# Kernel optimization log

Measured on AMD Instinct MI355X. Metric: run time of the kernel, lower is better.

The kernel has to match this reference:

```python
import jax, jax.numpy as jnp
import numpy as np

N_NODES = 100000


def gcn_conv(x, row, col, W, b, n_nodes):
    # PyG GCNConv: add self-loops, symmetric normalization, linear, scatter-add, bias
    deg = jnp.zeros((n_nodes,), x.dtype).at[col].add(1.0)
    dinv = jnp.where(deg > 0, jax.lax.rsqrt(deg), 0.0)
    norm = dinv[row] * dinv[col]                      # [E+N]
    h = x @ W                                         # [N, out]
    msg = h[row] * norm[:, None]                      # [E+N, out]
    out = jax.ops.segment_sum(msg, col, num_segments=n_nodes)
    return out + b


def setup_inputs() -> dict:
    key = jax.random.key(0)
    ks = jax.random.split(key, 8)
    E = 1600000
    edge_index = jax.random.randint(ks[0], (2, E), 0, N_NODES, dtype=jnp.int64)
    node_features = jax.random.normal(ks[1], (N_NODES, 16), dtype=jnp.float32)
    W1 = jax.random.normal(ks[2], (16, 32), dtype=jnp.float32) * 0.25
    b1 = jnp.zeros((32,), jnp.float32)
    W2 = jax.random.normal(ks[3], (32, 16), dtype=jnp.float32) * 0.18
    b2 = jnp.zeros((16,), jnp.float32)
    fc_W = jax.random.normal(ks[4], (16, 1), dtype=jnp.float32) * 0.25
    fc_b = jnp.zeros((1,), jnp.float32)
    return {"edge_index": edge_index, "node_features": node_features,
            "W1": W1, "b1": b1, "W2": W2, "b2": b2, "fc_W": fc_W, "fc_b": fc_b}


def reference(edge_index, node_features, W1, b1, W2, b2, fc_W, fc_b):
    n = node_features.shape[0]
    loops = jnp.arange(n, dtype=edge_index.dtype)
    row = jnp.concatenate([edge_index[0], loops])     # sources (with self-loops)
    col = jnp.concatenate([edge_index[1], loops])     # targets (with self-loops)
    x = jax.nn.relu(gcn_conv(node_features, row, col, W1, b1, n))
    # F.dropout with training=False is identity (inference)
    x = jax.nn.relu(gcn_conv(x, row, col, W2, b2, n))
    return x @ fc_W + fc_b
```

## Files before the change

### kernel.cpp

```cpp
#include <hip/hip_runtime.h>
#include <hip/hip_fp16.h>


constexpr int NN  = 100000;
constexpr int FIN = 16;
constexpr int FH  = 32;
constexpr int FO  = 16;

constexpr int BK      = 256;
constexpr int NBUCKET = (NN + BK - 1) / BK;
constexpr int CHUNK   = 8192;
constexpr int CAP     = 5632;

static __device__ __forceinline__ int pack2(float a, float b) {
    __half2 t = __float22half2_rn(make_float2(a, b));
    return *reinterpret_cast<int*>(&t);
}
static __device__ __forceinline__ float2 unpack2(int v) {
    __half2 t = *reinterpret_cast<__half2*>(&v);
    return __half22float2(t);
}

__global__ void init_kernel(int* __restrict__ bcursor,
                            __half* __restrict__ g1, __half* __restrict__ g2) {
    int b = blockIdx.x * blockDim.x + threadIdx.x;
    if (b < NBUCKET) bcursor[b] = b * CAP;
    if (b < 4) ((int4*)(g1 + (long long)NN * FH))[b] = make_int4(0, 0, 0, 0);
    else if (b < 6) ((int4*)(g2 + (long long)NN * FO))[b - 4] = make_int4(0, 0, 0, 0);
}

__global__ __launch_bounds__(512) void bucket_fill_kernel(
        const int* __restrict__ row, const int* __restrict__ col,
        int* __restrict__ bcursor, int* __restrict__ srow, int E) {
    __shared__ int bcnt[NBUCKET];
    __shared__ int bcur[NBUCKET];
    int t = threadIdx.x;
    int e0 = blockIdx.x * CHUNK;
    int m = E - e0; if (m > CHUNK) m = CHUNK;
    for (int b = t; b < NBUCKET; b += 512) bcnt[b] = 0;
    __syncthreads();
    for (int i = t; i < m; i += 512)
        atomicAdd(&bcnt[col[e0 + i] >> 8], 1);
    __syncthreads();
    for (int b = t; b < NBUCKET; b += 512) {
        int v = bcnt[b];
        bcur[b] = v ? atomicAdd(&bcursor[b], v) : 0;
    }
    __syncthreads();
    for (int i = t; i < m; i += 512) {
        int c = col[e0 + i];
        int r = row[e0 + i];
        int p = atomicAdd(&bcur[c >> 8], 1);
        srow[p] = ((c & (BK - 1)) << 17) | r;
    }
}

__global__ __launch_bounds__(512) void bucket_sort_mm1_kernel(
        const int* __restrict__ bcursor, int* __restrict__ srow,
        int* __restrict__ off, int* __restrict__ cnt, float* __restrict__ dinv,
        const float* __restrict__ x, const float* __restrict__ W1,
        __half* __restrict__ g1, int n) {
    __shared__ int ebuf[CAP];
    __shared__ int sorted[CAP];
    __shared__ int cnt2[BK];
    __shared__ float sdi[BK];
    __shared__ int wsum[4];
    __shared__ int wbase[4];
    __shared__ int Mtot;
    __shared__ float w1[FIN * FH];
    int t = threadIdx.x;
    for (int i = t; i < FIN * FH; i += 512) w1[i] = W1[i];
    int lo = blockIdx.x << 8;
    int nodes = n - lo; if (nodes > BK) nodes = BK;
    int s0 = blockIdx.x * CAP;
    int m = bcursor[blockIdx.x] - s0;
    if (m > CAP) m = CAP;
    if (m < 0)  m = 0;
    for (int i = t; i < m; i += 512) ebuf[i] = srow[s0 + i];
    if (t < BK) cnt2[t] = 0;
    __syncthreads();
    for (int i = t; i < m; i += 512) atomicAdd(&cnt2[ebuf[i] >> 17], 1);
    __syncthreads();
    int v = 0, pv = 0, s = 0, excl = 0;
    if (t < BK) {
        v  = cnt2[t];
        pv = (v + 3) & ~3;
        s  = pv;
        #pragma unroll
        for (int d = 1; d < 64; d <<= 1) {
            int u = __shfl_up(s, d, 64);
            if ((t & 63) >= d) s += u;
        }
        if ((t & 63) == 63) wsum[t >> 6] = s;
    }
    __syncthreads();
    if (t < 4) {
        int b = 0;
        for (int k = 0; k < t; k++) b += wsum[k];
        wbase[t] = b;
    }
    __syncthreads();
    if (t < BK) {
        excl = s + wbase[t >> 6] - pv;
        cnt2[t] = excl;
        float di = rsqrtf((float)v + 1.0f);
        sdi[t] = di;
        if (t < nodes) {
            off[lo + t]  = s0 + excl;
            cnt[lo + t]  = v;
            dinv[lo + t] = di;
        }
        if (t == BK - 1) Mtot = excl + pv;
    }
    __syncthreads();
    for (int i = t; i < m; i += 512) {
        int pvv = ebuf[i];
        int p = atomicAdd(&cnt2[pvv >> 17], 1);
        sorted[p] = pvv & 0x1FFFF;
    }
    __syncthreads();
    if (t < BK) {
        for (int p = excl + v; p < excl + pv; p++) sorted[p] = NN;
    }
    __syncthreads();
    int M = Mtot; if (M > CAP) M = CAP;
    for (int i = t; i < M; i += 512) srow[s0 + i] = sorted[i];
    int lane = t >> 8;
    int nd0  = t & 255;
    if (nd0 < nodes) {
        int nd = lo + nd0;
        float di = sdi[nd0];
        float xi[FIN];
        const float4* xv = (const float4*)(x + (long long)nd * FIN);
        #pragma unroll
        for (int i = 0; i < FIN / 4; i++) {
            float4 vv = xv[i];
            xi[4*i] = vv.x; xi[4*i+1] = vv.y; xi[4*i+2] = vv.z; xi[4*i+3] = vv.w;
        }
        float h[16];
        #pragma unroll
        for (int j = 0; j < 16; j++) h[j] = 0.f;
        const float* wl = w1 + lane * 16;
        #pragma unroll
        for (int i = 0; i < FIN; i++) {
            float xs = xi[i];
            #pragma unroll
            for (int j = 0; j < 16; j++) h[j] += xs * wl[i * FH + j];
        }
        int4* gv = (int4*)(g1 + (long long)nd * FH) + lane * 2;
        gv[0] = make_int4(pack2(h[0]*di,  h[1]*di),  pack2(h[2]*di,  h[3]*di),
                          pack2(h[4]*di,  h[5]*di),  pack2(h[6]*di,  h[7]*di));
        gv[1] = make_int4(pack2(h[8]*di,  h[9]*di),  pack2(h[10]*di, h[11]*di),
                          pack2(h[12]*di, h[13]*di), pack2(h[14]*di, h[15]*di));
    }
}

constexpr int XS = 36;
__global__ __launch_bounds__(256) void gather_mm2_kernel(
        const int* __restrict__ off, const int* __restrict__ cnt,
        const int* __restrict__ srow, const __half* __restrict__ g1,
        const float* __restrict__ dinv, const float* __restrict__ b1,
        const float* __restrict__ W2, __half* __restrict__ g2, int n) {
    __shared__ float xs[64 * XS];
    __shared__ float w[FH * FO];
    __shared__ float bb[FH];
    int t = threadIdx.x;
    for (int i = t; i < FH * FO; i += 256) w[i] = W2[i];
    if (t < FH) bb[t] = b1[t];
    int nl = t >> 2;
    int q = t & 3;
    int node = blockIdx.x * 64 + nl;
    bool live = node < n;
    float acc[8] = {0.f,0.f,0.f,0.f,0.f,0.f,0.f,0.f};
    float di = 0.f;
    if (live) {
        di = dinv[node];
        {
            int4 raw = ((const int4*)(g1 + (long long)node * FH))[q];
            float2 f0 = unpack2(raw.x), f1 = unpack2(raw.y);
            float2 f2 = unpack2(raw.z), f3 = unpack2(raw.w);
            acc[0] = f0.x; acc[1] = f0.y; acc[2] = f1.x; acc[3] = f1.y;
            acc[4] = f2.x; acc[5] = f2.y; acc[6] = f3.x; acc[7] = f3.y;
        }
        int s = off[node];
        int m = cnt[node];
        for (int i = 0; i < m; i += 4) {
            int4 ix = *(const int4*)(srow + s + i);
            int4 ra = ((const int4*)(g1 + (long long)ix.x * FH))[q];
            int4 rb = ((const int4*)(g1 + (long long)ix.y * FH))[q];
            int4 rc = ((const int4*)(g1 + (long long)ix.z * FH))[q];
            int4 rd = ((const int4*)(g1 + (long long)ix.w * FH))[q];
            float2 u;
            u = unpack2(ra.x); acc[0] += u.x; acc[1] += u.y;
            u = unpack2(ra.y); acc[2] += u.x; acc[3] += u.y;
            u = unpack2(ra.z); acc[4] += u.x; acc[5] += u.y;
            u = unpack2(ra.w); acc[6] += u.x; acc[7] += u.y;
            u = unpack2(rb.x); acc[0] += u.x; acc[1] += u.y;
            u = unpack2(rb.y); acc[2] += u.x; acc[3] += u.y;
            u = unpack2(rb.z); acc[4] += u.x; acc[5] += u.y;
            u = unpack2(rb.w); acc[6] += u.x; acc[7] += u.y;
            u = unpack2(rc.x); acc[0] += u.x; acc[1] += u.y;
            u = unpack2(rc.y); acc[2] += u.x; acc[3] += u.y;
            u = unpack2(rc.z); acc[4] += u.x; acc[5] += u.y;
            u = unpack2(rc.w); acc[6] += u.x; acc[7] += u.y;
            u = unpack2(rd.x); acc[0] += u.x; acc[1] += u.y;
            u = unpack2(rd.y); acc[2] += u.x; acc[3] += u.y;
            u = unpack2(rd.z); acc[4] += u.x; acc[5] += u.y;
            u = unpack2(rd.w); acc[6] += u.x; acc[7] += u.y;
        }
    }
    __syncthreads();
    if (live) {
        float* xr = xs + nl * XS + 8 * q;
        #pragma unroll
        for (int j = 0; j < 8; j++) {
            float a = acc[j] * di + bb[8*q + j];
            xr[j] = a > 0.f ? a : 0.f;
        }
    }
    __syncthreads();
    if (live) {
        const float* xr = xs + nl * XS;
        int k0 = 4 * q;
        float o0 = 0.f, o1 = 0.f, o2 = 0.f, o3 = 0.f;
        #pragma unroll
        for (int j = 0; j < FH; j++) {
            float xj = xr[j];
            const float* wr = w + j * FO + k0;
            o0 += xj * wr[0];
            o1 += xj * wr[1];
            o2 += xj * wr[2];
            o3 += xj * wr[3];
        }
        ((int2*)(g2 + (long long)node * FO))[q] =
            make_int2(pack2(o0 * di, o1 * di), pack2(o2 * di, o3 * di));
    }
}

__global__ __launch_bounds__(256) void gather_fc_kernel(
        const int* __restrict__ off, const int* __restrict__ cnt,
        const int* __restrict__ srow, const __half* __restrict__ g2,
        const float* __restrict__ dinv, const float* __restrict__ b2,
        const float* __restrict__ fcW, const float* __restrict__ fcb,
        float* __restrict__ out, int n) {
    __shared__ float w[FO];
    __shared__ float bb[FO];
    __shared__ float fb;
    int t = threadIdx.x;
    if (t < FO) { w[t] = fcW[t]; bb[t] = b2[t]; }
    if (t == 0) fb = fcb[0];
    __syncthreads();
    int node = blockIdx.x * 128 + (t >> 1);
    int q = t & 1;
    if (node >= n) return;
    float di = dinv[node];
    float acc[8];
    {
        int4 raw = ((const int4*)(g2 + (long long)node * FO))[q];
        float2 f0 = unpack2(raw.x), f1 = unpack2(raw.y);
        float2 f2 = unpack2(raw.z), f3 = unpack2(raw.w);
        acc[0] = f0.x; acc[1] = f0.y; acc[2] = f1.x; acc[3] = f1.y;
        acc[4] = f2.x; acc[5] = f2.y; acc[6] = f3.x; acc[7] = f3.y;
    }
    int s = off[node];
    int m = cnt[node];
    for (int i = 0; i < m; i += 4) {
        int4 ix = *(const int4*)(srow + s + i);
        int4 ra = ((const int4*)(g2 + (long long)ix.x * FO))[q];
        int4 rb = ((const int4*)(g2 + (long long)ix.y * FO))[q];
        int4 rc = ((const int4*)(g2 + (long long)ix.z * FO))[q];
        int4 rd = ((const int4*)(g2 + (long long)ix.w * FO))[q];
        float2 u;
        u = unpack2(ra.x); acc[0] += u.x; acc[1] += u.y;
        u = unpack2(ra.y); acc[2] += u.x; acc[3] += u.y;
        u = unpack2(ra.z); acc[4] += u.x; acc[5] += u.y;
        u = unpack2(ra.w); acc[6] += u.x; acc[7] += u.y;
        u = unpack2(rb.x); acc[0] += u.x; acc[1] += u.y;
        u = unpack2(rb.y); acc[2] += u.x; acc[3] += u.y;
        u = unpack2(rb.z); acc[4] += u.x; acc[5] += u.y;
        u = unpack2(rb.w); acc[6] += u.x; acc[7] += u.y;
        u = unpack2(rc.x); acc[0] += u.x; acc[1] += u.y;
        u = unpack2(rc.y); acc[2] += u.x; acc[3] += u.y;
        u = unpack2(rc.z); acc[4] += u.x; acc[5] += u.y;
        u = unpack2(rc.w); acc[6] += u.x; acc[7] += u.y;
        u = unpack2(rd.x); acc[0] += u.x; acc[1] += u.y;
        u = unpack2(rd.y); acc[2] += u.x; acc[3] += u.y;
        u = unpack2(rd.z); acc[4] += u.x; acc[5] += u.y;
        u = unpack2(rd.w); acc[6] += u.x; acc[7] += u.y;
    }
    float p = 0.f;
    #pragma unroll
    for (int j = 0; j < 8; j++) {
        float a = acc[j] * di + bb[8*q + j];
        p += (a > 0.f ? a : 0.f) * w[8*q + j];
    }
    p += __shfl_down(p, 1, 2);
    if (q == 0) out[node] = p + fb;
}

extern "C" void kernel_launch(void* const* d_in, const int* in_sizes, int n_in,
                              void* d_out, int out_size, void* d_ws, size_t ws_size,
                              hipStream_t stream) {
    const int*   edge = (const int*)d_in[0];
    const float* x    = (const float*)d_in[1];
    const float* W1   = (const float*)d_in[2];
    const float* b1   = (const float*)d_in[3];
    const float* W2   = (const float*)d_in[4];
    const float* b2   = (const float*)d_in[5];
    const float* fcW  = (const float*)d_in[6];
    const float* fcb  = (const float*)d_in[7];
    float* out = (float*)d_out;

    const int E = in_sizes[0] / 2;
    const int n = NN;
    const int* row = edge;
    const int* col = edge + E;

    const size_t nA = (size_t)((n + 127) & ~127);
    char* wsb = (char*)d_ws;
    int*   cnt     = (int*)wsb;
    int*   off     = cnt + nA;
    float* dinv    = (float*)(off + nA);
    int*   bcursor = (int*)(dinv + nA);
    int*   srow    = bcursor + 512;
    int*   srowEnd = srow + (size_t)(NBUCKET + 1) * CAP;
    __half* g1     = (__half*)srowEnd;
    __half* g2     = g1 + (size_t)(n + 1) * FH;

    const int nChunkBlocks = (E + CHUNK - 1) / CHUNK;

    init_kernel<<<2, 256, 0, stream>>>(bcursor, g1, g2);
    bucket_fill_kernel<<<nChunkBlocks, 512, 0, stream>>>(row, col, bcursor, srow, E);
    bucket_sort_mm1_kernel<<<NBUCKET, 512, 0, stream>>>(bcursor, srow, off, cnt, dinv, x, W1, g1, n);
    gather_mm2_kernel<<<(n + 63) / 64, 256, 0, stream>>>(off, cnt, srow, g1, dinv, b1, W2, g2, n);
    gather_fc_kernel<<<(n + 127) / 128, 256, 0, stream>>>(off, cnt, srow, g2, dinv, b2, fcW, fcb, out, n);
}
```

Baseline: 145.5 us.

## Aggregate raw 16-wide features before W1, fusing W1 and W2 into gather

Uses associativity to aggregate the dinv-scaled 16-dim input features over neighbors, then applies W1, bias, ReLU and W2 in the gather kernel. This halves the bytes gathered per edge in the first layer (16 halves instead of 32) and removes the separate W1 matmul pass and its shared-memory staging. Both gather loops are also unrolled to 8 edges per iteration for more memory-level parallelism. In exchange each node does the 16x32 and 32x16 matmuls in registers split across two lanes joined by a shuffle, which raises register pressure and the amount of compute per thread.

```diff
diff --git a/kernel.cpp b/kernel.cpp
--- a/kernel.cpp
+++ b/kernel.cpp
@@ -22,11 +22,11 @@
 }
 
 __global__ void init_kernel(int* __restrict__ bcursor,
-                            __half* __restrict__ g1, __half* __restrict__ g2) {
+                            __half* __restrict__ xd, __half* __restrict__ g2) {
     int b = blockIdx.x * blockDim.x + threadIdx.x;
     if (b < NBUCKET) bcursor[b] = b * CAP;
-    if (b < 4) ((int4*)(g1 + (long long)NN * FH))[b] = make_int4(0, 0, 0, 0);
-    else if (b < 6) ((int4*)(g2 + (long long)NN * FO))[b - 4] = make_int4(0, 0, 0, 0);
+    if (b < 2) ((int4*)(xd + (long long)NN * FIN))[b] = make_int4(0, 0, 0, 0);
+    else if (b < 4) ((int4*)(g2 + (long long)NN * FO))[b - 2] = make_int4(0, 0, 0, 0);
 }
 
 __global__ __launch_bounds__(512) void bucket_fill_kernel(
@@ -55,11 +55,10 @@
     }
 }
 
-__global__ __launch_bounds__(512) void bucket_sort_mm1_kernel(
+__global__ __launch_bounds__(512) void bucket_sort_scale_kernel(
         const int* __restrict__ bcursor, int* __restrict__ srow,
         int* __restrict__ off, int* __restrict__ cnt, float* __restrict__ dinv,
-        const float* __restrict__ x, const float* __restrict__ W1,
-        __half* __restrict__ g1, int n) {
+        const float* __restrict__ x, __half* __restrict__ xd, int n) {
     __shared__ int ebuf[CAP];
     __shared__ int sorted[CAP];
     __shared__ int cnt2[BK];
@@ -67,9 +66,7 @@
     __shared__ int wsum[4];
     __shared__ int wbase[4];
     __shared__ int Mtot;
-    __shared__ float w1[FIN * FH];
     int t = threadIdx.x;
-    for (int i = t; i < FIN * FH; i += 512) w1[i] = W1[i];
     int lo = blockIdx.x << 8;
     int nodes = n - lo; if (nodes > BK) nodes = BK;
     int s0 = blockIdx.x * CAP;
@@ -130,53 +127,36 @@
     if (nd0 < nodes) {
         int nd = lo + nd0;
         float di = sdi[nd0];
-        float xi[FIN];
-        const float4* xv = (const float4*)(x + (long long)nd * FIN);
-        #pragma unroll
-        for (int i = 0; i < FIN / 4; i++) {
-            float4 vv = xv[i];
-            xi[4*i] = vv.x; xi[4*i+1] = vv.y; xi[4*i+2] = vv.z; xi[4*i+3] = vv.w;
-        }
-        float h[16];
-        #pragma unroll
-        for (int j = 0; j < 16; j++) h[j] = 0.f;
-        const float* wl = w1 + lane * 16;
-        #pragma unroll
-        for (int i = 0; i < FIN; i++) {
-            float xs = xi[i];
-            #pragma unroll
-            for (int j = 0; j < 16; j++) h[j] += xs * wl[i * FH + j];
-        }
-        int4* gv = (int4*)(g1 + (long long)nd * FH) + lane * 2;
-        gv[0] = make_int4(pack2(h[0]*di,  h[1]*di),  pack2(h[2]*di,  h[3]*di),
-                          pack2(h[4]*di,  h[5]*di),  pack2(h[6]*di,  h[7]*di));
-        gv[1] = make_int4(pack2(h[8]*di,  h[9]*di),  pack2(h[10]*di, h[11]*di),
-                          pack2(h[12]*di, h[13]*di), pack2(h[14]*di, h[15]*di));
-    }
-}
-
-constexpr int XS = 36;
-__global__ __launch_bounds__(256) void gather_mm2_kernel(
+        const float4* xv = (const float4*)(x + (long long)nd * FIN) + lane * 2;
+        float4 v0 = xv[0], v1 = xv[1];
+        ((int4*)(xd + (long long)nd * FIN))[lane] =
+            make_int4(pack2(v0.x * di, v0.y * di), pack2(v0.z * di, v0.w * di),
+                      pack2(v1.x * di, v1.y * di), pack2(v1.z * di, v1.w * di));
+    }
+}
+
+__global__ __launch_bounds__(256) void gather1_kernel(
         const int* __restrict__ off, const int* __restrict__ cnt,
-        const int* __restrict__ srow, const __half* __restrict__ g1,
+        const int* __restrict__ srow, const __half* __restrict__ xd,
         const float* __restrict__ dinv, const float* __restrict__ b1,
-        const float* __restrict__ W2, __half* __restrict__ g2, int n) {
-    __shared__ float xs[64 * XS];
-    __shared__ float w[FH * FO];
+        const float* __restrict__ W1, const float* __restrict__ W2,
+        __half* __restrict__ g2, int n) {
+    __shared__ float w1[FIN * FH];
+    __shared__ float w2[FH * FO];
     __shared__ float bb[FH];
     int t = threadIdx.x;
-    for (int i = t; i < FH * FO; i += 256) w[i] = W2[i];
+    for (int i = t; i < FIN * FH; i += 256) w1[i] = W1[i];
+    for (int i = t; i < FH * FO; i += 256) w2[i] = W2[i];
     if (t < FH) bb[t] = b1[t];
-    int nl = t >> 2;
-    int q = t & 3;
-    int node = blockIdx.x * 64 + nl;
+    int node = blockIdx.x * 128 + (t >> 1);
+    int q = t & 1;
     bool live = node < n;
     float acc[8] = {0.f,0.f,0.f,0.f,0.f,0.f,0.f,0.f};
     float di = 0.f;
     if (live) {
         di = dinv[node];
         {
-            int4 raw = ((const int4*)(g1 + (long long)node * FH))[q];
+            int4 raw = ((const int4*)(xd + (long long)node * FIN))[q];
             float2 f0 = unpack2(raw.x), f1 = unpack2(raw.y);
             float2 f2 = unpack2(raw.z), f3 = unpack2(raw.w);
             acc[0] = f0.x; acc[1] = f0.y; acc[2] = f1.x; acc[3] = f1.y;
@@ -184,12 +164,18 @@
         }
         int s = off[node];
         int m = cnt[node];
-        for (int i = 0; i < m; i += 4) {
-            int4 ix = *(const int4*)(srow + s + i);
-            int4 ra = ((const int4*)(g1 + (long long)ix.x * FH))[q];
-            int4 rb = ((const int4*)(g1 + (long long)ix.y * FH))[q];
-            int4 rc = ((const int4*)(g1 + (long long)ix.z * FH))[q];
-            int4 rd = ((const int4*)(g1 + (long long)ix.w * FH))[q];
+        int i = 0;
+        for (; i + 7 < m; i += 8) {
+            int4 ix0 = *(const int4*)(srow + s + i);
+            int4 ix1 = *(const int4*)(srow + s + i + 4);
+            int4 ra = ((const int4*)(xd + (long long)ix0.x * FIN))[q];
+            int4 rb = ((const int4*)(xd + (long long)ix0.y * FIN))[q];
+            int4 rc = ((const int4*)(xd + (long long)ix0.z * FIN))[q];
+            int4 rd = ((const int4*)(xd + (long long)ix0.w * FIN))[q];
+            int4 re = ((const int4*)(xd + (long long)ix1.x * FIN))[q];
+            int4 rf = ((const int4*)(xd + (long long)ix1.y * FIN))[q];
+            int4 rg = ((const int4*)(xd + (long long)ix1.z * FIN))[q];
+            int4 rh = ((const int4*)(xd + (long long)ix1.w * FIN))[q];
             float2 u;
             u = unpack2(ra.x); acc[0] += u.x; acc[1] += u.y;
             u = unpack2(ra.y); acc[2] += u.x; acc[3] += u.y;
@@ -207,33 +193,79 @@
             u = unpack2(rd.y); acc[2] += u.x; acc[3] += u.y;
             u = unpack2(rd.z); acc[4] += u.x; acc[5] += u.y;
             u = unpack2(rd.w); acc[6] += u.x; acc[7] += u.y;
+            u = unpack2(re.x); acc[0] += u.x; acc[1] += u.y;
+            u = unpack2(re.y); acc[2] += u.x; acc[3] += u.y;
+            u = unpack2(re.z); acc[4] += u.x; acc[5] += u.y;
+            u = unpack2(re.w); acc[6] += u.x; acc[7] += u.y;
+            u = unpack2(rf.x); acc[0] += u.x; acc[1] += u.y;
+            u = unpack2(rf.y); acc[2] += u.x; acc[3] += u.y;
+            u = unpack2(rf.z); acc[4] += u.x; acc[5] += u.y;
+            u = unpack2(rf.w); acc[6] += u.x; acc[7] += u.y;
+            u = unpack2(rg.x); acc[0] += u.x; acc[1] += u.y;
+            u = unpack2(rg.y); acc[2] += u.x; acc[3] += u.y;
+            u = unpack2(rg.z); acc[4] += u.x; acc[5] += u.y;
+            u = unpack2(rg.w); acc[6] += u.x; acc[7] += u.y;
+            u = unpack2(rh.x); acc[0] += u.x; acc[1] += u.y;
+            u = unpack2(rh.y); acc[2] += u.x; acc[3] += u.y;
+            u = unpack2(rh.z); acc[4] += u.x; acc[5] += u.y;
+            u = unpack2(rh.w); acc[6] += u.x; acc[7] += u.y;
+        }
+        for (; i < m; i += 4) {
+            int4 ix = *(const int4*)(srow + s + i);
+            int4 ra = ((const int4*)(xd + (long long)ix.x * FIN))[q];
+            int4 rb = ((const int4*)(xd + (long long)ix.y * FIN))[q];
+            int4 rc = ((const int4*)(xd + (long long)ix.z * FIN))[q];
+            int4 rd = ((const int4*)(xd + (long long)ix.w * FIN))[q];
+            float2 u;
+            u = unpack2(ra.x); acc[0] += u.x; acc[1] += u.y;
+            u = unpack2(ra.y); acc[2] += u.x; acc[3] += u.y;
+            u = unpack2(ra.z); acc[4] += u.x; acc[5] += u.y;
+            u = unpack2(ra.w); acc[6] += u.x; acc[7] += u.y;
+            u = unpack2(rb.x); acc[0] += u.x; acc[1] += u.y;
+            u = unpack2(rb.y); acc[2] += u.x; acc[3] += u.y;
+            u = unpack2(rb.z); acc[4] += u.x; acc[5] += u.y;
+            u = unpack2(rb.w); acc[6] += u.x; acc[7] += u.y;
+            u = unpack2(rc.x); acc[0] += u.x; acc[1] += u.y;
+            u = unpack2(rc.y); acc[2] += u.x; acc[3] += u.y;
+            u = unpack2(rc.z); acc[4] += u.x; acc[5] += u.y;
+            u = unpack2(rc.w); acc[6] += u.x; acc[7] += u.y;
+            u = unpack2(rd.x); acc[0] += u.x; acc[1] += u.y;
+            u = unpack2(rd.y); acc[2] += u.x; acc[3] += u.y;
+            u = unpack2(rd.z); acc[4] += u.x; acc[5] += u.y;
+            u = unpack2(rd.w); acc[6] += u.x; acc[7] += u.y;
         }
     }
     __syncthreads();
     if (live) {
-        float* xr = xs + nl * XS + 8 * q;
+        float a[FIN];
         #pragma unroll
         for (int j = 0; j < 8; j++) {
-            float a = acc[j] * di + bb[8*q + j];
-            xr[j] = a > 0.f ? a : 0.f;
-        }
-    }
-    __syncthreads();
-    if (live) {
-        const float* xr = xs + nl * XS;
-        int k0 = 4 * q;
-        float o0 = 0.f, o1 = 0.f, o2 = 0.f, o3 = 0.f;
+            float o = __shfl_xor(acc[j], 1);
+            a[8 * q + j] = acc[j];
+            a[8 * (1 - q) + j] = o;
+        }
+        float o[FO];
         #pragma unroll
-        for (int j = 0; j < FH; j++) {
-            float xj = xr[j];
-            const float* wr = w + j * FO + k0;
-            o0 += xj * wr[0];
-            o1 += xj * wr[1];
-            o2 += xj * wr[2];
-            o3 += xj * wr[3];
-        }
-        ((int2*)(g2 + (long long)node * FO))[q] =
-            make_int2(pack2(o0 * di, o1 * di), pack2(o2 * di, o3 * di));
+        for (int kk = 0; kk < FO; kk++) o[kk] = 0.f;
+        int k0 = 16 * q;
+        #pragma unroll
+        for (int k = 0; k < 16; k++) {
+            float h = 0.f;
+            #pragma unroll
+            for (int i2 = 0; i2 < FIN; i2++) h += a[i2] * w1[i2 * FH + k0 + k];
+            float x1 = h * di + bb[k0 + k];
+            x1 = x1 > 0.f ? x1 : 0.f;
+            const float* wr = w2 + (k0 + k) * FO;
+            #pragma unroll
+            for (int kk = 0; kk < FO; kk++) o[kk] += x1 * wr[kk];
+        }
+        #pragma unroll
+        for (int kk = 0; kk < FO; kk++) o[kk] += __shfl_xor(o[kk], 1);
+        ((int4*)(g2 + (long long)node * FO))[q] =
+            make_int4(pack2(o[8*q]   * di, o[8*q+1] * di),
+                      pack2(o[8*q+2] * di, o[8*q+3] * di),
+                      pack2(o[8*q+4] * di, o[8*q+5] * di),
+                      pack2(o[8*q+6] * di, o[8*q+7] * di));
     }
 }
 
@@ -264,7 +296,53 @@
     }
     int s = off[node];
     int m = cnt[node];
-    for (int i = 0; i < m; i += 4) {
+    int i = 0;
+    for (; i + 7 < m; i += 8) {
+        int4 ix0 = *(const int4*)(srow + s + i);
+        int4 ix1 = *(const int4*)(srow + s + i + 4);
+        int4 ra = ((const int4*)(g2 + (long long)ix0.x * FO))[q];
+        int4 rb = ((const int4*)(g2 + (long long)ix0.y * FO))[q];
+        int4 rc = ((const int4*)(g2 + (long long)ix0.z * FO))[q];
+        int4 rd = ((const int4*)(g2 + (long long)ix0.w * FO))[q];
+        int4 re = ((const int4*)(g2 + (long long)ix1.x * FO))[q];
+        int4 rf = ((const int4*)(g2 + (long long)ix1.y * FO))[q];
+        int4 rg = ((const int4*)(g2 + (long long)ix1.z * FO))[q];
+        int4 rh = ((const int4*)(g2 + (long long)ix1.w * FO))[q];
+        float2 u;
+        u = unpack2(ra.x); acc[0] += u.x; acc[1] += u.y;
+        u = unpack2(ra.y); acc[2] += u.x; acc[3] += u.y;
+        u = unpack2(ra.z); acc[4] += u.x; acc[5] += u.y;
+        u = unpack2(ra.w); acc[6] += u.x; acc[7] += u.y;
+        u = unpack2(rb.x); acc[0] += u.x; acc[1] += u.y;
+        u = unpack2(rb.y); acc[2] += u.x; acc[3] += u.y;
+        u = unpack2(rb.z); acc[4] += u.x; acc[5] += u.y;
+        u = unpack2(rb.w); acc[6] += u.x; acc[7] += u.y;
+        u = unpack2(rc.x); acc[0] += u.x; acc[1] += u.y;
+        u = unpack2(rc.y); acc[2] += u.x; acc[3] += u.y;
+        u = unpack2(rc.z); acc[4] += u.x; acc[5] += u.y;
+        u = unpack2(rc.w); acc[6] += u.x; acc[7] += u.y;
+        u = unpack2(rd.x); acc[0] += u.x; acc[1] += u.y;
+        u = unpack2(rd.y); acc[2] += u.x; acc[3] += u.y;
+        u = unpack2(rd.z); acc[4] += u.x; acc[5] += u.y;
+        u = unpack2(rd.w); acc[6] += u.x; acc[7] += u.y;
+        u = unpack2(re.x); acc[0] += u.x; acc[1] += u.y;
+        u = unpack2(re.y); acc[2] += u.x; acc[3] += u.y;
+        u = unpack2(re.z); acc[4] += u.x; acc[5] += u.y;
+        u = unpack2(re.w); acc[6] += u.x; acc[7] += u.y;
+        u = unpack2(rf.x); acc[0] += u.x; acc[1] += u.y;
+        u = unpack2(rf.y); acc[2] += u.x; acc[3] += u.y;
+        u = unpack2(rf.z); acc[4] += u.x; acc[5] += u.y;
+        u = unpack2(rf.w); acc[6] += u.x; acc[7] += u.y;
+        u = unpack2(rg.x); acc[0] += u.x; acc[1] += u.y;
+        u = unpack2(rg.y); acc[2] += u.x; acc[3] += u.y;
+        u = unpack2(rg.z); acc[4] += u.x; acc[5] += u.y;
+        u = unpack2(rg.w); acc[6] += u.x; acc[7] += u.y;
+        u = unpack2(rh.x); acc[0] += u.x; acc[1] += u.y;
+        u = unpack2(rh.y); acc[2] += u.x; acc[3] += u.y;
+        u = unpack2(rh.z); acc[4] += u.x; acc[5] += u.y;
+        u = unpack2(rh.w); acc[6] += u.x; acc[7] += u.y;
+    }
+    for (; i < m; i += 4) {
         int4 ix = *(const int4*)(srow + s + i);
         int4 ra = ((const int4*)(g2 + (long long)ix.x * FO))[q];
         int4 rb = ((const int4*)(g2 + (long long)ix.y * FO))[q];
@@ -324,14 +402,14 @@
     int*   bcursor = (int*)(dinv + nA);
     int*   srow    = bcursor + 512;
     int*   srowEnd = srow + (size_t)(NBUCKET + 1) * CAP;
-    __half* g1     = (__half*)srowEnd;
-    __half* g2     = g1 + (size_t)(n + 1) * FH;
+    __half* xd     = (__half*)srowEnd;
+    __half* g2     = xd + (size_t)(n + 1) * FIN;
 
     const int nChunkBlocks = (E + CHUNK - 1) / CHUNK;
 
-    init_kernel<<<2, 256, 0, stream>>>(bcursor, g1, g2);
+    init_kernel<<<2, 256, 0, stream>>>(bcursor, xd, g2);
     bucket_fill_kernel<<<nChunkBlocks, 512, 0, stream>>>(row, col, bcursor, srow, E);
-    bucket_sort_mm1_kernel<<<NBUCKET, 512, 0, stream>>>(bcursor, srow, off, cnt, dinv, x, W1, g1, n);
-    gather_mm2_kernel<<<(n + 63) / 64, 256, 0, stream>>>(off, cnt, srow, g1, dinv, b1, W2, g2, n);
+    bucket_sort_scale_kernel<<<NBUCKET, 512, 0, stream>>>(bcursor, srow, off, cnt, dinv, x, xd, n);
+    gather1_kernel<<<(n + 127) / 128, 256, 0, stream>>>(off, cnt, srow, xd, dinv, b1, W1, W2, g2, n);
     gather_fc_kernel<<<(n + 127) / 128, 256, 0, stream>>>(off, cnt, srow, g2, dinv, b2, fcW, fcb, out, n);
 }
```

New measurement: 148.2 us. No clear change (+1.8%).
